# Kernel optimization log

Measured on AMD Instinct MI355X. Metric: run time of the kernel, lower is better.

Reference implementation:

```python
import jax, jax.numpy as jnp
import numpy as np

I16_MIN, I16_MAX = -32768, 32767
NUM_SEG = 8


def setup_inputs() -> dict:
    key = jax.random.key(0)
    k1, k2, k3, k4, k5, k6 = jax.random.split(key, 6)
    # Float activation; quantized to qint16 inside the op via input_scale.
    x = jax.random.normal(k1, (16, 1024, 2048), dtype=jnp.float32)
    input_scale = jnp.full((1,), 1.0 / 8192.0, dtype=jnp.float32)  # randn*8192 spans most of int16
    out_scale = jnp.full((1,), 1e-3, dtype=jnp.float32)
    # Per-segment fixed-point linear coefficients (as produced by _convert_linear_kb / toqint):
    # 16-bit k, wide b pre-shifted by left_shift, result right-shifted by right_shift.
    alpha = jax.random.randint(k2, (NUM_SEG,), -4096, 4096, dtype=jnp.int32)        # int16 k
    beta = jax.random.randint(k3, (NUM_SEG,), -(1 << 20), 1 << 20, dtype=jnp.int32)  # int b
    left_shift = jax.random.randint(k4, (NUM_SEG,), 0, 5, dtype=jnp.int32)           # int8 shift
    right_shift = jax.random.randint(k5, (NUM_SEG,), 1, 15, dtype=jnp.int32)         # int8 shift
    # Sorted segment upper bounds in quantized domain; last entry pinned to qint16 max
    # (mirrors `segment_max[-1] = info.max` in _init_multi_table_params).
    segment_max = jnp.sort(jax.random.randint(k6, (NUM_SEG,), I16_MIN, I16_MAX, dtype=jnp.int32))
    segment_max = segment_max.at[-1].set(I16_MAX)
    return dict(x=x, input_scale=input_scale, out_scale=out_scale, alpha=alpha,
                beta=beta, left_shift=left_shift, right_shift=right_shift,
                segment_max=segment_max)


def reference(x, input_scale, out_scale, alpha, beta, left_shift, right_shift, segment_max):
    # Quantize input to qint16 (scale-only, zero_point = 0 as in the module).
    xi = jnp.clip(jnp.round(x / input_scale), I16_MIN, I16_MAX).astype(jnp.int32)
    # Segment selection: element belongs to the first segment whose upper bound >= xi.
    idx = jnp.clip(jnp.searchsorted(segment_max, xi, side='left'), 0, NUM_SEG - 1)
    # Gather per-segment fixed-point coefficients.
    k = alpha[idx]
    b = beta[idx]
    ls = left_shift[idx]
    rs = right_shift[idx]
    # Hardware shift-multiply-add: acc = k*x + (b << left_shift), then rounded
    # arithmetic right shift by right_shift, saturate to qint16.
    acc = k * xi + jnp.left_shift(b, ls)
    round_bias = jnp.where(rs > 0, jnp.left_shift(jnp.int32(1), jnp.maximum(rs - 1, 0)), jnp.int32(0))
    qy = jnp.clip(jnp.right_shift(acc + round_bias, rs), I16_MIN, I16_MAX)
    # Dequantized output (QTensor data * out_scale, zero_point = 0).
    return qy.astype(jnp.float32) * out_scale
```

## Files before the change

### kernel.cpp

```cpp
#include <hip/hip_runtime.h>


#define SEG_I16_MIN (-32768)
#define SEG_I16_MAX (32767)

__device__ __forceinline__ float seg_one(float x, float s, float os,
                                         int sm0, int sm1, int sm2, int sm3,
                                         int sm4, int sm5, int sm6,
                                         const int4* tab)
{
    float xf = x / s;
    xf = rintf(xf);
    xf = fminf(fmaxf(xf, -32768.0f), 32767.0f);
    int xi = (int)xf;
    int idx = (sm0 < xi) + (sm1 < xi) + (sm2 < xi) + (sm3 < xi)
            + (sm4 < xi) + (sm5 < xi) + (sm6 < xi);
    int4 t = tab[idx];
    int acc = t.x * xi + t.y;
    int qy = acc >> t.z;
    qy = min(max(qy, SEG_I16_MIN), SEG_I16_MAX);
    return (float)qy * os;
}

__global__ __launch_bounds__(256) void SegmentLUT_83021717831949_kernel(
    const float* __restrict__ x,
    const float* __restrict__ input_scale,
    const float* __restrict__ out_scale,
    const int*   __restrict__ alpha,
    const int*   __restrict__ beta,
    const int*   __restrict__ lsh,
    const int*   __restrict__ rsh,
    const int*   __restrict__ smax,
    float*       __restrict__ out,
    int n)
{
    __shared__ int4 tab[8];
    if (threadIdx.x < 8) {
        int j  = (int)threadIdx.x;
        int rs = rsh[j];
        int rm1 = rs - 1 > 0 ? rs - 1 : 0;
        int rbias = rs > 0 ? (1 << rm1) : 0;
        int bc = (int)((unsigned)beta[j] << (lsh[j] & 31)) + rbias;
        tab[j] = make_int4(alpha[j], bc, rs, 0);
    }
    float s  = input_scale[0];
    float os = out_scale[0];
    int sm0 = smax[0], sm1 = smax[1], sm2 = smax[2], sm3 = smax[3];
    int sm4 = smax[4], sm5 = smax[5], sm6 = smax[6];
    __syncthreads();

    int nvec   = n >> 2;
    int stride = (int)(gridDim.x * blockDim.x);
    int tid    = (int)(blockIdx.x * blockDim.x + threadIdx.x);

    const float4* __restrict__ xv = (const float4*)x;
    float4* __restrict__ ov = (float4*)out;

    for (int i = tid; i < nvec; i += stride) {
        float4 v = xv[i];
        float4 o;
        o.x = seg_one(v.x, s, os, sm0, sm1, sm2, sm3, sm4, sm5, sm6, tab);
        o.y = seg_one(v.y, s, os, sm0, sm1, sm2, sm3, sm4, sm5, sm6, tab);
        o.z = seg_one(v.z, s, os, sm0, sm1, sm2, sm3, sm4, sm5, sm6, tab);
        o.w = seg_one(v.w, s, os, sm0, sm1, sm2, sm3, sm4, sm5, sm6, tab);
        ov[i] = o;
    }
    for (int i = (nvec << 2) + tid; i < n; i += stride) {
        out[i] = seg_one(x[i], s, os, sm0, sm1, sm2, sm3, sm4, sm5, sm6, tab);
    }
}

extern "C" void kernel_launch(void* const* d_in, const int* in_sizes, int n_in,
                              void* d_out, int out_size, void* d_ws, size_t ws_size,
                              hipStream_t stream) {
    const float* x           = (const float*)d_in[0];
    const float* input_scale = (const float*)d_in[1];
    const float* out_scale   = (const float*)d_in[2];
    const int*   alpha       = (const int*)d_in[3];
    const int*   beta        = (const int*)d_in[4];
    const int*   lsh         = (const int*)d_in[5];
    const int*   rsh         = (const int*)d_in[6];
    const int*   smax        = (const int*)d_in[7];
    float* out = (float*)d_out;

    int n = in_sizes[0];
    int nvec = n >> 2;
    int blocks = (nvec + 255) / 256;
    if (blocks > 2048) blocks = 2048;
    if (blocks < 1) blocks = 1;

    SegmentLUT_83021717831949_kernel<<<blocks, 256, 0, stream>>>(
        x, input_scale, out_scale, alpha, beta, lsh, rsh, smax, out, n);
}
```

Measured before the change: 243.2 us.

## Replace integer fixed-point segment math with float FMA and unroll loop by two

Folds the right shift and output scale into per-segment float slope and intercept, so each element needs one FMA and a clamp instead of an integer multiply, shift, clamp and float convert. The divide by input scale becomes a multiply by its reciprocal, and segment comparisons run in float. The grid-stride loop is unrolled to issue two float4 loads per iteration. This drops the exact floor-shift rounding and can differ from the integer reference near rounding boundaries, and the reciprocal multiply may round differently from a true divide.

Result: no change. 245.3 us (+0.9%).

```diff
diff --git a/kernel.cpp b/kernel.cpp
--- a/kernel.cpp
+++ b/kernel.cpp
@@ -1,25 +1,18 @@
 #include <hip/hip_runtime.h>
 
 
-#define SEG_I16_MIN (-32768)
-#define SEG_I16_MAX (32767)
-
-__device__ __forceinline__ float seg_one(float x, float s, float os,
-                                         int sm0, int sm1, int sm2, int sm3,
-                                         int sm4, int sm5, int sm6,
-                                         const int4* tab)
+__device__ __forceinline__ float seg_one(float x, float inv_s,
+                                         float sm0, float sm1, float sm2, float sm3,
+                                         float sm4, float sm5, float sm6,
+                                         const float2* tab, float olo, float ohi)
 {
-    float xf = x / s;
-    xf = rintf(xf);
+    float xf = rintf(x * inv_s);
     xf = fminf(fmaxf(xf, -32768.0f), 32767.0f);
-    int xi = (int)xf;
-    int idx = (sm0 < xi) + (sm1 < xi) + (sm2 < xi) + (sm3 < xi)
-            + (sm4 < xi) + (sm5 < xi) + (sm6 < xi);
-    int4 t = tab[idx];
-    int acc = t.x * xi + t.y;
-    int qy = acc >> t.z;
-    qy = min(max(qy, SEG_I16_MIN), SEG_I16_MAX);
-    return (float)qy * os;
+    int idx = (sm0 < xf) + (sm1 < xf) + (sm2 < xf) + (sm3 < xf)
+            + (sm4 < xf) + (sm5 < xf) + (sm6 < xf);
+    float2 t = tab[idx];
+    float y = fmaf(t.x, xf, t.y);
+    return fminf(fmaxf(y, olo), ohi);
 }
 
 __global__ __launch_bounds__(256) void SegmentLUT_83021717831949_kernel(
@@ -34,19 +27,23 @@
     float*       __restrict__ out,
     int n)
 {
-    __shared__ int4 tab[8];
+    __shared__ float2 tab[8];
+    float os = out_scale[0];
     if (threadIdx.x < 8) {
         int j  = (int)threadIdx.x;
         int rs = rsh[j];
         int rm1 = rs - 1 > 0 ? rs - 1 : 0;
         int rbias = rs > 0 ? (1 << rm1) : 0;
         int bc = (int)((unsigned)beta[j] << (lsh[j] & 31)) + rbias;
-        tab[j] = make_int4(alpha[j], bc, rs, 0);
+        float sc = ldexpf(os, -rs);
+        tab[j] = make_float2((float)alpha[j] * sc, (float)bc * sc);
     }
-    float s  = input_scale[0];
-    float os = out_scale[0];
-    int sm0 = smax[0], sm1 = smax[1], sm2 = smax[2], sm3 = smax[3];
-    int sm4 = smax[4], sm5 = smax[5], sm6 = smax[6];
+    float s     = input_scale[0];
+    float inv_s = 1.0f / s;
+    float sm0 = (float)smax[0], sm1 = (float)smax[1], sm2 = (float)smax[2];
+    float sm3 = (float)smax[3], sm4 = (float)smax[4], sm5 = (float)smax[5];
+    float sm6 = (float)smax[6];
+    float olo = -32768.0f * os, ohi = 32767.0f * os;
     __syncthreads();
 
     int nvec   = n >> 2;
@@ -56,17 +53,33 @@
     const float4* __restrict__ xv = (const float4*)x;
     float4* __restrict__ ov = (float4*)out;
 
-    for (int i = tid; i < nvec; i += stride) {
-        float4 v = xv[i];
-        float4 o;
-        o.x = seg_one(v.x, s, os, sm0, sm1, sm2, sm3, sm4, sm5, sm6, tab);
-        o.y = seg_one(v.y, s, os, sm0, sm1, sm2, sm3, sm4, sm5, sm6, tab);
-        o.z = seg_one(v.z, s, os, sm0, sm1, sm2, sm3, sm4, sm5, sm6, tab);
-        o.w = seg_one(v.w, s, os, sm0, sm1, sm2, sm3, sm4, sm5, sm6, tab);
-        ov[i] = o;
+    int i = tid;
+    for (; i + stride < nvec; i += 2 * stride) {
+        float4 a = xv[i];
+        float4 b = xv[i + stride];
+        float4 oa, ob;
+        oa.x = seg_one(a.x, inv_s, sm0, sm1, sm2, sm3, sm4, sm5, sm6, tab, olo, ohi);
+        oa.y = seg_one(a.y, inv_s, sm0, sm1, sm2, sm3, sm4, sm5, sm6, tab, olo, ohi);
+        oa.z = seg_one(a.z, inv_s, sm0, sm1, sm2, sm3, sm4, sm5, sm6, tab, olo, ohi);
+        oa.w = seg_one(a.w, inv_s, sm0, sm1, sm2, sm3, sm4, sm5, sm6, tab, olo, ohi);
+        ob.x = seg_one(b.x, inv_s, sm0, sm1, sm2, sm3, sm4, sm5, sm6, tab, olo, ohi);
+        ob.y = seg_one(b.y, inv_s, sm0, sm1, sm2, sm3, sm4, sm5, sm6, tab, olo, ohi);
+        ob.z = seg_one(b.z, inv_s, sm0, sm1, sm2, sm3, sm4, sm5, sm6, tab, olo, ohi);
+        ob.w = seg_one(b.w, inv_s, sm0, sm1, sm2, sm3, sm4, sm5, sm6, tab, olo, ohi);
+        ov[i] = oa;
+        ov[i + stride] = ob;
     }
-    for (int i = (nvec << 2) + tid; i < n; i += stride) {
-        out[i] = seg_one(x[i], s, os, sm0, sm1, sm2, sm3, sm4, sm5, sm6, tab);
+    for (; i < nvec; i += stride) {
+        float4 a = xv[i];
+        float4 oa;
+        oa.x = seg_one(a.x, inv_s, sm0, sm1, sm2, sm3, sm4, sm5, sm6, tab, olo, ohi);
+        oa.y = seg_one(a.y, inv_s, sm0, sm1, sm2, sm3, sm4, sm5, sm6, tab, olo, ohi);
+        oa.z = seg_one(a.z, inv_s, sm0, sm1, sm2, sm3, sm4, sm5, sm6, tab, olo, ohi);
+        oa.w = seg_one(a.w, inv_s, sm0, sm1, sm2, sm3, sm4, sm5, sm6, tab, olo, ohi);
+        ov[i] = oa;
+    }
+    for (int k = (nvec << 2) + tid; k < n; k += stride) {
+        out[k] = seg_one(x[k], inv_s, sm0, sm1, sm2, sm3, sm4, sm5, sm6, tab, olo, ohi);
     }
 }
 
```
